# Kernel optimization log

Hardware: AMD Instinct MI355X
Metric: run time of the kernel (lower is better)

Reference implementation:

```python
import jax, jax.numpy as jnp
import numpy as np


def _lstm_cell(x, h, c, Wih, Whh, bih, bhh):
    # PyTorch LSTMCell gate order: i, f, g, o
    g = x @ Wih.T + h @ Whh.T + bih + bhh
    i, f, gg, o = jnp.split(g, 4, axis=-1)
    c = jax.nn.sigmoid(f) * c + jax.nn.sigmoid(i) * jnp.tanh(gg)
    h = jax.nn.sigmoid(o) * jnp.tanh(c)
    return h, c


def setup_inputs() -> dict:
    F, H, B, Te, Td = 64, 128, 1024, 168, 24
    shapes = {
        'input_p_q': (B, Te, F), 'label_p': (B, Td),
        'Wi_w': (H, F), 'Wi_b': (H,), 'We_w': (H, 2 * H),
        'Vd_w': (F, H), 'Vd_b': (F,),
        'enc_Wih': (4 * H, F), 'enc_Whh': (4 * H, H), 'enc_bih': (4 * H,), 'enc_bhh': (4 * H,),
        'mid_Wih': (4 * H, H), 'mid_Whh': (4 * H, H), 'mid_bih': (4 * H,), 'mid_bhh': (4 * H,),
        'Wx_w': (H, H), 'Wx_b': (H,), 'Wh_w': (H, 2 * H),
        'V_w': (1, H), 'V_b': (1,),
        'dec_Wih': (4 * H, H), 'dec_Whh': (4 * H, H), 'dec_bih': (4 * H,), 'dec_bhh': (4 * H,),
        'reg_w': (1, H), 'reg_b': (1,),
    }
    key = jax.random.key(0)
    ks = jax.random.split(key, len(shapes))
    out = {}
    for k, (name, shp) in zip(ks, shapes.items()):
        scale = 1.0 if name in ('input_p_q', 'label_p') else 0.05
        out[name] = jax.random.normal(k, shp, jnp.float32) * scale
    return out


def reference(input_p_q, label_p, Wi_w, Wi_b, We_w, Vd_w, Vd_b,
              enc_Wih, enc_Whh, enc_bih, enc_bhh,
              mid_Wih, mid_Whh, mid_bih, mid_bhh,
              Wx_w, Wx_b, Wh_w, V_w, V_b,
              dec_Wih, dec_Whh, dec_bih, dec_bhh, reg_w, reg_b):
    B, Te, F = input_p_q.shape
    H = Wi_w.shape[0]
    Td = label_p.shape[1]
    h0 = jnp.zeros((B, H), input_p_q.dtype)

    # ---- spatial-attention LSTMCell encoder ----
    xs = jnp.transpose(input_p_q, (1, 0, 2))  # [Te, B, F]

    def enc_step(carry, x_t):
        h, c = carry
        s = jnp.tanh(jnp.concatenate([h, c], axis=1) @ We_w.T
                     + x_t @ Wi_w.T + Wi_b) @ Vd_w.T + Vd_b  # [B, F]
        x_in = x_t * jax.nn.softmax(s, axis=1)
        h, c = _lstm_cell(x_in, h, c, enc_Wih, enc_Whh, enc_bih, enc_bhh)
        return (h, c), h

    _, mid = jax.lax.scan(enc_step, (h0, h0), xs)  # [Te, B, H]

    # ---- single-layer nn.LSTM (LSTM_mid), zero init state ----
    def mid_step(carry, x_t):
        h, c = carry
        h, c = _lstm_cell(x_t, h, c, mid_Wih, mid_Whh, mid_bih, mid_bhh)
        return (h, c), h

    (hi, ci), mid_out = jax.lax.scan(mid_step, (h0, h0), mid)
    mid_out = jnp.transpose(mid_out, (1, 0, 2))  # [B, Te, H]

    # ---- temporal-attention LSTMCell decoder (no softmax on scores, faithful) ----
    wx_mid = mid_out @ Wx_w.T + Wx_b  # [B, Te, H]

    def dec_step(carry, _):
        hi, ci = carry
        q = jnp.concatenate([hi, ci], axis=1) @ Wh_w.T  # [B, H]
        s = jnp.tanh(q[:, None, :] + wx_mid) @ V_w.T + V_b  # [B, Te, 1]
        dec_in = jnp.einsum('bt,bth->bh', s[..., 0], mid_out)
        hi, ci = _lstm_cell(dec_in, hi, ci, dec_Wih, dec_Whh, dec_bih, dec_bhh)
        return (hi, ci), hi

    _, dec = jax.lax.scan(dec_step, (hi, ci), None, length=Td)  # [Td, B, H]
    out = jnp.transpose(dec, (1, 0, 2)) @ reg_w.T + reg_b  # [B, Td, 1]
    return out[..., 0]
```

## Files before the change

kernel.cpp:

```cpp
#include <hip/hip_runtime.h>

#define B_   1024
#define TE   168
#define TD   24
#define F_   64
#define H_   128
#define H2_  256
#define G_   512

#define OFF_WhT    0
#define OFF_dWihT  16384
#define OFF_dWhhT  49152
#define OFF_ENCB   81920
#define OFF_MIDB   82432
#define OFF_DECB   82944
#define OFF_W16    83456
#define W16_We     0
#define W16_Wi     32768
#define W16_Vd     40960
#define W16_eWih   49152
#define W16_eWhh   81920
#define W16_mWih   147456
#define W16_mWhh   212992
#define W16_Wx     278528
#define W16_TOT    294912
#define OFF_MID    230912
#define OFF_WX     (OFF_MID + (B_*TE*H_)/2)
#define OFF_STH    (OFF_WX  + (B_*TE*H_)/2)
#define OFF_STC    (OFF_STH + B_*H_)
#define WS_FLOATS  (OFF_STC + B_*H_)

typedef _Float16 h2 __attribute__((ext_vector_type(2)));
typedef _Float16 h8 __attribute__((ext_vector_type(8)));
typedef _Float16 f16x8 __attribute__((ext_vector_type(8)));
typedef float    f32x4 __attribute__((ext_vector_type(4)));

__device__ __forceinline__ float fexp2(float x) { return __builtin_amdgcn_exp2f(x); }
__device__ __forceinline__ float frcp(float x)  { return __builtin_amdgcn_rcpf(x); }
#define LOG2E 1.4426950408889634f

__device__ __forceinline__ float sigm(float x) {
    return frcp(1.f + fexp2(-LOG2E * x));
}
__device__ __forceinline__ float tanh_fast(float x) {
    float e = fexp2(2.f * LOG2E * x);
    return 1.f - 2.f * frcp(e + 1.f);
}

__device__ __forceinline__ float fdot2(h2 a, h2 b, float c) {
#if __has_builtin(__builtin_amdgcn_fdot2)
    return __builtin_amdgcn_fdot2(a, b, c, false);
#else
    return c + (float)a[0] * (float)b[0] + (float)a[1] * (float)b[1];
#endif
}
__device__ __forceinline__ void fma4(float4& g, const float4 wv, const float s) {
    g.x = __builtin_fmaf(wv.x, s, g.x);
    g.y = __builtin_fmaf(wv.y, s, g.y);
    g.z = __builtin_fmaf(wv.z, s, g.z);
    g.w = __builtin_fmaf(wv.w, s, g.w);
}

#define SH(V,I)  __builtin_shufflevector(V, V, 2*(I), 2*(I)+1)
#define SL(CG)   (4*((CG) + ((CG)>>3)))

#define DPAIR2(LOV, HIV, R0, R1) { \
    h2 c0=SH(LOV,0), c1=SH(LOV,1), c2=SH(LOV,2), c3=SH(LOV,3); \
    h2 c4=SH(HIV,0), c5=SH(HIV,1), c6=SH(HIV,2), c7=SH(HIV,3); \
    a00.x=fdot2(R0,c0,a00.x); a00.y=fdot2(R0,c1,a00.y); a00.z=fdot2(R0,c2,a00.z); a00.w=fdot2(R0,c3,a00.w); \
    a01.x=fdot2(R0,c4,a01.x); a01.y=fdot2(R0,c5,a01.y); a01.z=fdot2(R0,c6,a01.z); a01.w=fdot2(R0,c7,a01.w); \
    a10.x=fdot2(R1,c0,a10.x); a10.y=fdot2(R1,c1,a10.y); a10.z=fdot2(R1,c2,a10.z); a10.w=fdot2(R1,c3,a10.w); \
    a11.x=fdot2(R1,c4,a11.x); a11.y=fdot2(R1,c5,a11.y); a11.z=fdot2(R1,c6,a11.z); a11.w=fdot2(R1,c7,a11.w); \
}

__device__ __forceinline__ f32x4 mfma16(f16x8 a, f16x8 b, f32x4 c) {
    return __builtin_amdgcn_mfma_f32_16x16x32_f16(a, b, c, 0, 0, 0);
}

struct PrepArgs {
    const float *We, *Wi, *Vd, *eWih, *eWhh, *eBih, *eBhh,
                *mWih, *mWhh, *mBih, *mBhh, *Wx, *Wh, *dWih, *dWhh, *dBih, *dBhh;
};

__global__ void prep_kernel(PrepArgs a, float* __restrict__ ws, int* __restrict__ flags) {
    int sec  = blockIdx.x >> 2;
    int base = (blockIdx.x & 3) * blockDim.x + threadIdx.x;
    const int stride = blockDim.x * 4;
    _Float16* w16 = (_Float16*)(ws + OFF_W16);

    if (sec <= 2) {
        const float* src = (sec == 0) ? a.Wh : (sec == 1) ? a.dWih : a.dWhh;
        int R = (sec == 0) ? 128 : 512;
        int C = (sec == 0) ? 256 : 128;
        int off = (sec == 0) ? OFF_WhT : (sec == 1) ? OFF_dWihT : OFF_dWhhT;
        int n = R * C;
        _Float16* hd = (_Float16*)(ws + off);
        for (int o = base; o < n; o += stride) {
            int r = o % R, c = o / R;
            hd[(c >> 1) * 2 * R + 2 * r + (c & 1)] = (_Float16)src[r * C + c];
        }
    } else if (sec == 3) {
        for (int i = base; i < 512; i += stride) ws[OFF_ENCB + i] = a.eBih[i] + a.eBhh[i];
    } else if (sec == 4) {
        for (int i = base; i < 512; i += stride) ws[OFF_MIDB + i] = a.mBih[i] + a.mBhh[i];
    } else if (sec == 5) {
        for (int i = base; i < 512; i += stride) ws[OFF_DECB + i] = a.dBih[i] + a.dBhh[i];
        for (int i = base; i < 64; i += stride) flags[i] = 0;
    } else if (sec <= 13) {
        const int dsto[8] = {W16_We, W16_Wi, W16_Vd, W16_eWih, W16_eWhh, W16_mWih, W16_mWhh, W16_Wx};
        const int cnt[8]  = {32768, 8192, 8192, 32768, 65536, 65536, 65536, 16384};
        const float* srcs[8] = {a.We, a.Wi, a.Vd, a.eWih, a.eWhh, a.mWih, a.mWhh, a.Wx};
        int k = sec - 6;
        const float* s = srcs[k];
        _Float16* d = w16 + dsto[k];
        int n = cnt[k];
        for (int i = base; i < n; i += stride) d[i] = (_Float16)s[i];
    }
}

__global__ __launch_bounds__(512, 1) void enc_mid_kernel(
    const float* __restrict__ x_all,
    const float* __restrict__ Wi_b,
    const float* __restrict__ Vd_b,
    const float* __restrict__ Wx_b,
    float* __restrict__ ws,
    int* __restrict__ flags)
{
    const int tid  = threadIdx.x;
    const int wave = tid >> 6;
    const int lane = tid & 63;
    const int g    = lane >> 4;
    const int cc   = lane & 15;
    const int role = blockIdx.x >> 6;
    const int grp  = blockIdx.x & 63;
    const int b0   = grp * 16;
    const int col  = wave * 16 + cc;
    const _Float16* w16 = (const _Float16*)(ws + OFF_W16);
    _Float16* hencG = (_Float16*)(ws + OFF_MID);

    if (role == 0) {
        __shared__ __align__(16) _Float16 m1In[16][328];
        __shared__ __align__(16) _Float16 encIn[16][200];
        __shared__ __align__(16) _Float16 avT[16][136];
        __shared__ __align__(16) float sS[16][68];
        __shared__ __align__(16) float xf[16][64];
        __shared__ __align__(16) float cE[16][132];
        __shared__ float bWi[H_], bVd[F_], bE[G_];

        for (int i = tid; i < 16 * 328; i += 512) ((_Float16*)m1In)[i]  = (_Float16)0.f;
        for (int i = tid; i < 16 * 200; i += 512) ((_Float16*)encIn)[i] = (_Float16)0.f;
        for (int i = tid; i < 16 * 132; i += 512) ((float*)cE)[i] = 0.f;
        if (tid < H_) bWi[tid] = Wi_b[tid];
        if (tid < F_) bVd[tid] = Vd_b[tid];
        bE[tid] = ws[OFF_ENCB + tid];
        if (tid < 256) {
            int m = tid >> 4, c4 = (tid & 15) * 4;
            float4 v = *(const float4*)&x_all[((size_t)(b0 + m) * TE + 0) * F_ + c4];
            *(float4*)&xf[m][c4] = v;
            m1In[m][256 + c4]     = (_Float16)v.x;
            m1In[m][256 + c4 + 1] = (_Float16)v.y;
            m1In[m][256 + c4 + 2] = (_Float16)v.z;
            m1In[m][256 + c4 + 3] = (_Float16)v.w;
        }

        f16x8 wWe[8], wWi[2], wVd[4], wIh[4][2], wHh[4][4];
        {
            const _Float16* p = w16 + W16_We + (size_t)col * 256 + 8 * g;
            #pragma unroll
            for (int ks = 0; ks < 8; ++ks) wWe[ks] = *(const f16x8*)(p + ks * 32);
            const _Float16* p2 = w16 + W16_Wi + (size_t)col * 64 + 8 * g;
            wWi[0] = *(const f16x8*)(p2);
            wWi[1] = *(const f16x8*)(p2 + 32);
            if (wave < 4) {
                const _Float16* p3 = w16 + W16_Vd + (size_t)col * 128 + 8 * g;
                #pragma unroll
                for (int ks = 0; ks < 4; ++ks) wVd[ks] = *(const f16x8*)(p3 + ks * 32);
            } else {
                #pragma unroll
                for (int ks = 0; ks < 4; ++ks) wVd[ks] = f16x8{};
            }
            #pragma unroll
            for (int q = 0; q < 4; ++q) {
                const _Float16* pi = w16 + W16_eWih + (size_t)(q * 128 + col) * 64 + 8 * g;
                wIh[q][0] = *(const f16x8*)(pi);
                wIh[q][1] = *(const f16x8*)(pi + 32);
                const _Float16* ph = w16 + W16_eWhh + (size_t)(q * 128 + col) * 128 + 8 * g;
                #pragma unroll
                for (int ks = 0; ks < 4; ++ks) wHh[q][ks] = *(const f16x8*)(ph + ks * 32);
            }
        }
        __syncthreads();

        float4 xr = make_float4(0.f, 0.f, 0.f, 0.f);

        for (int t = 0; t < TE; ++t) {
            {
                f16x8 aF[10];
                #pragma unroll
                for (int ks = 0; ks < 10; ++ks)
                    aF[ks] = *(const f16x8*)&m1In[cc][ks * 32 + 8 * g];
                f32x4 acc = {0.f, 0.f, 0.f, 0.f};
                #pragma unroll
                for (int ks = 0; ks < 8; ++ks)
                    acc = mfma16(aF[ks], wWe[ks], acc);
                acc = mfma16(aF[8], wWi[0], acc);
                acc = mfma16(aF[9], wWi[1], acc);
                float bw = bWi[col];
                #pragma unroll
                for (int r = 0; r < 4; ++r)
                    avT[4 * g + r][col] = (_Float16)tanh_fast(acc[r] + bw);
            }
            __syncthreads();

            if (wave < 4) {
                f16x8 aF[4];
                #pragma unroll
                for (int ks = 0; ks < 4; ++ks)
                    aF[ks] = *(const f16x8*)&avT[cc][ks * 32 + 8 * g];
                f32x4 acc = {0.f, 0.f, 0.f, 0.f};
                #pragma unroll
                for (int ks = 0; ks < 4; ++ks)
                    acc = mfma16(aF[ks], wVd[ks], acc);
                float bv = bVd[col];
                #pragma unroll
                for (int r = 0; r < 4; ++r)
                    sS[4 * g + r][col] = acc[r] + bv;
            } else if (t + 1 < TE) {
                int q = tid - 256, m = q >> 4, c4 = (q & 15) * 4;
                xr = *(const float4*)&x_all[((size_t)(b0 + m) * TE + (t + 1)) * F_ + c4];
            }
            __syncthreads();

            {
                int m = tid >> 5, c = tid & 31;
                float v0 = sS[m][c], v1 = sS[m][c + 32];
                float mx = fmaxf(v0, v1);
                #pragma unroll
                for (int off = 16; off > 0; off >>= 1) mx = fmaxf(mx, __shfl_xor(mx, off, 64));
                float e0 = fexp2((v0 - mx) * LOG2E);
                float e1 = fexp2((v1 - mx) * LOG2E);
                float sm = e0 + e1;
                #pragma unroll
                for (int off = 16; off > 0; off >>= 1) sm += __shfl_xor(sm, off, 64);
                float rs = frcp(sm);
                encIn[m][c]      = (_Float16)(xf[m][c]      * e0 * rs);
                encIn[m][c + 32] = (_Float16)(xf[m][c + 32] * e1 * rs);
            }
            __syncthreads();

            f32x4 ge[4];
            {
                f16x8 aF[6];
                #pragma unroll
                for (int ks = 0; ks < 6; ++ks)
                    aF[ks] = *(const f16x8*)&encIn[cc][ks * 32 + 8 * g];
                #pragma unroll
                for (int q = 0; q < 4; ++q) {
                    f32x4 acc = {0.f, 0.f, 0.f, 0.f};
                    acc = mfma16(aF[0], wIh[q][0], acc);
                    acc = mfma16(aF[1], wIh[q][1], acc);
                    #pragma unroll
                    for (int ks = 0; ks < 4; ++ks)
                        acc = mfma16(aF[2 + ks], wHh[q][ks], acc);
                    ge[q] = acc;
                }
            }
            __syncthreads();
            {
                float bi = bE[col], bf = bE[col + 128], bg = bE[col + 256], bo = bE[col + 384];
                #pragma unroll
                for (int r = 0; r < 4; ++r) {
                    int m = 4 * g + r;
                    float gi = ge[0][r] + bi, gf = ge[1][r] + bf,
                          gg = ge[2][r] + bg, go = ge[3][r] + bo;
                    float cn = sigm(gf) * cE[m][col] + sigm(gi) * tanh_fast(gg);
                    float h  = sigm(go) * tanh_fast(cn);
                    cE[m][col] = cn;
                    _Float16 hh = (_Float16)h;
                    encIn[m][64 + col] = hh;
                    m1In[m][col]       = hh;
                    m1In[m][128 + col] = (_Float16)cn;
                    hencG[((size_t)(b0 + m) * TE + t) * H_ + col] = hh;
                }
                if (tid >= 256 && t + 1 < TE) {
                    int q = tid - 256, m = q >> 4, c4 = (q & 15) * 4;
                    *(float4*)&xf[m][c4] = xr;
                    m1In[m][256 + c4]     = (_Float16)xr.x;
                    m1In[m][256 + c4 + 1] = (_Float16)xr.y;
                    m1In[m][256 + c4 + 2] = (_Float16)xr.z;
                    m1In[m][256 + c4 + 3] = (_Float16)xr.w;
                }
            }
            __syncthreads();
            if (((t + 1) & 7) == 0 && tid == 0)
                __hip_atomic_store(flags + grp, t + 1, __ATOMIC_RELEASE, __HIP_MEMORY_SCOPE_AGENT);
        }
    } else {
        __shared__ __align__(16) _Float16 midIn[16][264];
        __shared__ __align__(16) float cM[16][132];
        __shared__ float bM[G_], bWx[H_];

        for (int i = tid; i < 16 * 264; i += 512) ((_Float16*)midIn)[i] = (_Float16)0.f;
        for (int i = tid; i < 16 * 132; i += 512) ((float*)cM)[i] = 0.f;
        if (tid < H_) bWx[tid] = Wx_b[tid];
        bM[tid] = ws[OFF_MIDB + tid];

        f16x8 wIhB[4][4], wHhB[4][4], wWx[4];
        {
            #pragma unroll
            for (int q = 0; q < 4; ++q) {
                const _Float16* pi = w16 + W16_mWih + (size_t)(q * 128 + col) * 128 + 8 * g;
                const _Float16* ph = w16 + W16_mWhh + (size_t)(q * 128 + col) * 128 + 8 * g;
                #pragma unroll
                for (int ks = 0; ks < 4; ++ks) {
                    wIhB[q][ks] = *(const f16x8*)(pi + ks * 32);
                    wHhB[q][ks] = *(const f16x8*)(ph + ks * 32);
                }
            }
            const _Float16* px = w16 + W16_Wx + (size_t)col * 128 + 8 * g;
            #pragma unroll
            for (int ks = 0; ks < 4; ++ks) wWx[ks] = *(const f16x8*)(px + ks * 32);
        }
        _Float16* wxH = (_Float16*)(ws + OFF_WX);
        __syncthreads();

        if (tid == 0) {
            while (__hip_atomic_load(flags + grp, __ATOMIC_ACQUIRE, __HIP_MEMORY_SCOPE_AGENT) < 8)
                __builtin_amdgcn_s_sleep(4);
        }
        __syncthreads();
        if (tid < 256) {
            int m = tid >> 4, s8 = (tid & 15) * 8;
            *(f16x8*)&midIn[m][s8] = *(const f16x8*)&hencG[((size_t)(b0 + m) * TE + 0) * H_ + s8];
        }
        __syncthreads();

        f16x8 hpre = {};
        f32x4 accx = {0.f, 0.f, 0.f, 0.f};

        for (int t = 0; t < TE; ++t) {
            const bool pre_ok = (t + 1 < TE) && (((t + 1) & 7) != 0);
            f32x4 gm[4];
            {
                f16x8 aF[8];
                #pragma unroll
                for (int ks = 0; ks < 8; ++ks)
                    aF[ks] = *(const f16x8*)&midIn[cc][ks * 32 + 8 * g];
                #pragma unroll
                for (int q = 0; q < 4; ++q) {
                    f32x4 acc = {0.f, 0.f, 0.f, 0.f};
                    #pragma unroll
                    for (int ks = 0; ks < 4; ++ks)
                        acc = mfma16(aF[ks], wIhB[q][ks], acc);
                    #pragma unroll
                    for (int ks = 0; ks < 4; ++ks)
                        acc = mfma16(aF[4 + ks], wHhB[q][ks], acc);
                    gm[q] = acc;
                }
                if (t > 0) {
                    f32x4 acc = {0.f, 0.f, 0.f, 0.f};
                    #pragma unroll
                    for (int ks = 0; ks < 4; ++ks)
                        acc = mfma16(aF[4 + ks], wWx[ks], acc);
                    accx = acc;
                }
            }
            if (tid < 256 && pre_ok) {
                int m = tid >> 4, s8 = (tid & 15) * 8;
                hpre = *(const f16x8*)&hencG[((size_t)(b0 + m) * TE + (t + 1)) * H_ + s8];
            }
            __syncthreads();

            {
                float bi = bM[col], bf = bM[col + 128], bg = bM[col + 256], bo = bM[col + 384];
                float bw = bWx[col];
                #pragma unroll
                for (int r = 0; r < 4; ++r) {
                    int m = 4 * g + r;
                    float gi = gm[0][r] + bi, gf = gm[1][r] + bf,
                          gg = gm[2][r] + bg, go = gm[3][r] + bo;
                    float cn = sigm(gf) * cM[m][col] + sigm(gi) * tanh_fast(gg);
                    float h  = sigm(go) * tanh_fast(cn);
                    cM[m][col] = cn;
                    _Float16 hh = (_Float16)h;
                    midIn[m][128 + col] = hh;
                    hencG[((size_t)(b0 + m) * TE + t) * H_ + col] = hh;
                    if (t > 0)
                        wxH[((size_t)(b0 + m) * TE + (t - 1)) * H_ + col] = (_Float16)(accx[r] + bw);
                }
                if (tid < 256 && pre_ok) {
                    int m = tid >> 4, s8 = (tid & 15) * 8;
                    *(f16x8*)&midIn[m][s8] = hpre;
                }
            }
            __syncthreads();

            if (t + 1 < TE && ((t + 1) & 7) == 0) {
                if (tid == 0) {
                    while (__hip_atomic_load(flags + grp, __ATOMIC_ACQUIRE, __HIP_MEMORY_SCOPE_AGENT) < t + 9)
                        __builtin_amdgcn_s_sleep(4);
                }
                __syncthreads();
                if (tid < 256) {
                    int m = tid >> 4, s8 = (tid & 15) * 8;
                    *(f16x8*)&midIn[m][s8] = *(const f16x8*)&hencG[((size_t)(b0 + m) * TE + (t + 1)) * H_ + s8];
                }
                __syncthreads();
            }
        }

        {
            f16x8 ax[4];
            #pragma unroll
            for (int ks = 0; ks < 4; ++ks)
                ax[ks] = *(const f16x8*)&midIn[cc][128 + ks * 32 + 8 * g];
            f32x4 acc = {0.f, 0.f, 0.f, 0.f};
            #pragma unroll
            for (int ks = 0; ks < 4; ++ks)
                acc = mfma16(ax[ks], wWx[ks], acc);
            float bw = bWx[col];
            #pragma unroll
            for (int r = 0; r < 4; ++r) {
                int m = 4 * g + r;
                wxH[((size_t)(b0 + m) * TE + (TE - 1)) * H_ + col] = (_Float16)(acc[r] + bw);
            }
        }
        for (int idx = tid; idx < 2048; idx += 512) {
            int m = idx >> 7, j = idx & 127;
            ws[OFF_STH + (b0 + m) * H_ + j] = (float)midIn[m][128 + j];
            ws[OFF_STC + (b0 + m) * H_ + j] = cM[m][j];
        }
    }
}

#define QP_ 132

__global__ __launch_bounds__(512, 2) void dec_kernel(
    const float* __restrict__ Vw_in,
    const float* __restrict__ Vb_in,
    const float* __restrict__ rw_in,
    const float* __restrict__ rb_in,
    const float* __restrict__ ws,
    float* __restrict__ out)
{
    __shared__ __align__(16) float scr[9216];
    __shared__ __align__(16) float hc2[2][H2_];
    __shared__ __align__(16) float qv[2][QP_];
    __shared__ __align__(16) float sb[2][TE];
    __shared__ __align__(16) float dinp[8][2][H_];
    __shared__ float bD[G_], Vw[H_], rw[H_];

    const int tid = threadIdx.x;
    const int b0  = blockIdx.x * 2;
    const float Vb = Vb_in[0], rb = rb_in[0];

    {
        int r = tid >> 8, c = tid & 255;
        hc2[r][c] = (c < H_) ? ws[OFF_STH + (b0 + r) * H_ + c]
                             : ws[OFF_STC + (b0 + r) * H_ + (c - H_)];
    }
    if (tid < H_) { Vw[tid] = Vw_in[tid]; rw[tid] = rw_in[tid]; }
    bD[tid] = ws[OFF_DECB + tid];
    __syncthreads();

    const h8* WhH2  = (const h8*)(ws + OFF_WhT);
    const h8* dWih2 = (const h8*)(ws + OFF_dWihT);
    const h8* dWhh2 = (const h8*)(ws + OFF_dWhhT);
    const h8* wx8   = (const h8*)(ws + OFF_WX);
    typedef _Float16 h4 __attribute__((ext_vector_type(4)));
    const h4* mid4 = (const h4*)(ws + OFF_MID);

    for (int td = 0; td < TD; ++td) {
        {
            int cg = tid & 15, ks = tid >> 4;
            int p0 = ks * 4;
            float4 a00 = make_float4(0.f,0.f,0.f,0.f), a01 = a00, a10 = a00, a11 = a00;
            #pragma unroll
            for (int i = 0; i < 4; ++i) {
                int p = p0 + i;
                h8 lo = WhH2[p * 32 + cg * 2];
                h8 hi = WhH2[p * 32 + cg * 2 + 1];
                h2 r0; r0[0] = (_Float16)hc2[0][2*p]; r0[1] = (_Float16)hc2[0][2*p+1];
                h2 r1; r1[0] = (_Float16)hc2[1][2*p]; r1[1] = (_Float16)hc2[1][2*p+1];
                DPAIR2(lo, hi, r0, r1);
            }
            int sl = SL(cg);
            float* sp = scr + ks * 288;
            *(float4*)(sp +       sl) = a00; *(float4*)(sp +  72 + sl) = a01;
            *(float4*)(sp + 144 + sl) = a10; *(float4*)(sp + 216 + sl) = a11;
        }
        __syncthreads();
        if (tid < 256) {
            int j = tid & 127, r = tid >> 7;
            int e = j & 7, cgj = j >> 3;
            int idx = r * 144 + ((e < 4) ? SL(cgj) + e : 72 + SL(cgj) + (e - 4));
            float v = 0.f;
            #pragma unroll
            for (int ks = 0; ks < 32; ++ks) v += scr[ks * 288 + idx];
            qv[r][j] = v;
        }
        __syncthreads();

        for (int task = tid; task < 2 * TE; task += 512) {
            int r = (task >= TE) ? 1 : 0;
            int tp = task - r * TE;
            const h8* wxr = wx8 + ((size_t)(b0 + r) * TE + tp) * 16;
            float acc = Vb;
            #pragma unroll 4
            for (int kk = 0; kk < 16; ++kk) {
                h8 hv = wxr[kk];
                int j = kk * 8;
                float4 q0 = *(const float4*)&qv[r][j], q1 = *(const float4*)&qv[r][j + 4];
                float4 v0 = *(const float4*)&Vw[j],    v1 = *(const float4*)&Vw[j + 4];
                acc += tanh_fast(q0.x + (float)hv[0]) * v0.x + tanh_fast(q0.y + (float)hv[1]) * v0.y
                     + tanh_fast(q0.z + (float)hv[2]) * v0.z + tanh_fast(q0.w + (float)hv[3]) * v0.w;
                acc += tanh_fast(q1.x + (float)hv[4]) * v1.x + tanh_fast(q1.y + (float)hv[5]) * v1.y
                     + tanh_fast(q1.z + (float)hv[6]) * v1.z + tanh_fast(q1.w + (float)hv[7]) * v1.w;
            }
            sb[r][tp] = acc;
        }
        __syncthreads();

        {
            int ts = tid >> 6, r = (tid >> 5) & 1, cg = tid & 31;
            int t0 = ts * 21;
            float4 a = make_float4(0.f, 0.f, 0.f, 0.f);
            #pragma unroll 3
            for (int tp = t0; tp < t0 + 21; ++tp) {
                float s = sb[r][tp];
                h4 m = mid4[((size_t)(b0 + r) * TE + tp) * 32 + cg];
                float4 mf;
                mf.x = (float)m[0]; mf.y = (float)m[1]; mf.z = (float)m[2]; mf.w = (float)m[3];
                fma4(a, mf, s);
            }
            *(float4*)&dinp[ts][r][cg * 4] = a;
        }
        __syncthreads();
        if (tid < 256) {
            int j = tid & 127, r = tid >> 7;
            qv[r][j] = ((dinp[0][r][j] + dinp[1][r][j]) + (dinp[2][r][j] + dinp[3][r][j]))
                     + ((dinp[4][r][j] + dinp[5][r][j]) + (dinp[6][r][j] + dinp[7][r][j]));
        }
        __syncthreads();

        {
            int cg = tid & 63, ks = tid >> 6;
            int p0 = ks * 8;
            float4 a00 = make_float4(0.f,0.f,0.f,0.f), a01 = a00, a10 = a00, a11 = a00;
            #pragma unroll 4
            for (int i = 0; i < 8; ++i) {
                int p = p0 + i;
                h8 lo = dWih2[p * 128 + cg * 2];
                h8 hi = dWih2[p * 128 + cg * 2 + 1];
                h2 r0; r0[0] = (_Float16)qv[0][2*p]; r0[1] = (_Float16)qv[0][2*p+1];
                h2 r1; r1[0] = (_Float16)qv[1][2*p]; r1[1] = (_Float16)qv[1][2*p+1];
                DPAIR2(lo, hi, r0, r1);
            }
            #pragma unroll 4
            for (int i = 0; i < 8; ++i) {
                int p = p0 + i;
                h8 lo = dWhh2[p * 128 + cg * 2];
                h8 hi = dWhh2[p * 128 + cg * 2 + 1];
                h2 r0; r0[0] = (_Float16)hc2[0][2*p]; r0[1] = (_Float16)hc2[0][2*p+1];
                h2 r1; r1[0] = (_Float16)hc2[1][2*p]; r1[1] = (_Float16)hc2[1][2*p+1];
                DPAIR2(lo, hi, r0, r1);
            }
            int sl = SL(cg);
            float* sp = scr + ks * 1152;
            *(float4*)(sp +       sl) = a00; *(float4*)(sp + 288 + sl) = a01;
            *(float4*)(sp + 576 + sl) = a10; *(float4*)(sp + 864 + sl) = a11;
        }
        __syncthreads();

        if (tid < 256) {
            int j = tid & 127, r = tid >> 7;
            int e = j & 7, cgj = j >> 3;
            int i0, i1, i2, i3;
            {
                int c0 = cgj, c1 = 16 + cgj, c2 = 32 + cgj, c3 = 48 + cgj;
                i0 = (e < 4) ? SL(c0) + e : 288 + SL(c0) + (e - 4);
                i1 = (e < 4) ? SL(c1) + e : 288 + SL(c1) + (e - 4);
                i2 = (e < 4) ? SL(c2) + e : 288 + SL(c2) + (e - 4);
                i3 = (e < 4) ? SL(c3) + e : 288 + SL(c3) + (e - 4);
            }
            const float* sp = scr + r * 576;
            float gi = bD[j], gf = bD[j + 128], gg = bD[j + 256], go = bD[j + 384];
            #pragma unroll
            for (int ks = 0; ks < 8; ++ks) {
                const float* p = sp + ks * 1152;
                gi += p[i0]; gf += p[i1]; gg += p[i2]; go += p[i3];
            }
            float c = sigm(gf) * hc2[r][H_ + j] + sigm(gi) * tanh_fast(gg);
            float h = sigm(go) * tanh_fast(c);
            hc2[r][H_ + j] = c; hc2[r][j] = h;
        }
        __syncthreads();

        if (tid < 128) {
            int r = tid >> 6, lane = tid & 63;
            float v = hc2[r][lane] * rw[lane] + hc2[r][lane + 64] * rw[lane + 64];
            for (int off = 32; off > 0; off >>= 1) v += __shfl_xor(v, off, 64);
            if (lane == 0) out[(b0 + r) * TD + td] = v + rb;
        }
    }
}

extern "C" void kernel_launch(void* const* d_in, const int* in_sizes, int n_in,
                              void* d_out, int out_size, void* d_ws, size_t ws_size,
                              hipStream_t stream)
{
    (void)in_sizes; (void)n_in; (void)out_size;
    if (ws_size < (size_t)WS_FLOATS * sizeof(float)) return;

    const float* x_all = (const float*)d_in[0];
    const float* Wi_b  = (const float*)d_in[3];
    const float* Vd_b  = (const float*)d_in[6];
    const float* Wx_b  = (const float*)d_in[16];
    const float* V_w   = (const float*)d_in[18];
    const float* V_b   = (const float*)d_in[19];
    const float* reg_w = (const float*)d_in[24];
    const float* reg_b = (const float*)d_in[25];
    float* ws  = (float*)d_ws;
    float* out = (float*)d_out;
    int* flags = (int*)d_out;

    PrepArgs pa{
        (const float*)d_in[4],
        (const float*)d_in[2],
        (const float*)d_in[5],
        (const float*)d_in[7],
        (const float*)d_in[8],
        (const float*)d_in[9],
        (const float*)d_in[10],
        (const float*)d_in[11],
        (const float*)d_in[12],
        (const float*)d_in[13],
        (const float*)d_in[14],
        (const float*)d_in[15],
        (const float*)d_in[17],
        (const float*)d_in[20],
        (const float*)d_in[21],
        (const float*)d_in[22],
        (const float*)d_in[23]
    };

    prep_kernel<<<56, 256, 0, stream>>>(pa, ws, flags);
    enc_mid_kernel<<<128, 512, 0, stream>>>(x_all, Wi_b, Vd_b, Wx_b, ws, flags);
    dec_kernel<<<512, 512, 0, stream>>>(V_w, V_b, reg_w, reg_b, ws, out);
}
```

Baseline: 1.079 ms.

## Fuse attention softmax into Vd MFMA waves and double-buffer encoder input

Result: slower. 1.395 ms (+29.3%).

```diff
diff --git a/kernel.cpp b/kernel.cpp
--- a/kernel.cpp
+++ b/kernel.cpp
@@ -140,15 +140,14 @@
 
     if (role == 0) {
         __shared__ __align__(16) _Float16 m1In[16][328];
-        __shared__ __align__(16) _Float16 encIn[16][200];
+        __shared__ __align__(16) _Float16 encIn[2][16][200];
         __shared__ __align__(16) _Float16 avT[16][136];
-        __shared__ __align__(16) float sS[16][68];
         __shared__ __align__(16) float xf[16][64];
         __shared__ __align__(16) float cE[16][132];
         __shared__ float bWi[H_], bVd[F_], bE[G_];
 
         for (int i = tid; i < 16 * 328; i += 512) ((_Float16*)m1In)[i]  = (_Float16)0.f;
-        for (int i = tid; i < 16 * 200; i += 512) ((_Float16*)encIn)[i] = (_Float16)0.f;
+        for (int i = tid; i < 2 * 16 * 200; i += 512) ((_Float16*)encIn)[i] = (_Float16)0.f;
         for (int i = tid; i < 16 * 132; i += 512) ((float*)cE)[i] = 0.f;
         if (tid < H_) bWi[tid] = Wi_b[tid];
         if (tid < F_) bVd[tid] = Vd_b[tid];
@@ -163,7 +162,7 @@
             m1In[m][256 + c4 + 3] = (_Float16)v.w;
         }
 
-        f16x8 wWe[8], wWi[2], wVd[4], wIh[4][2], wHh[4][4];
+        f16x8 wWe[8], wWi[2], wVd[4][4], wIh[4][2], wHh[4][4];
         {
             const _Float16* p = w16 + W16_We + (size_t)col * 256 + 8 * g;
             #pragma unroll
@@ -172,12 +171,17 @@
             wWi[0] = *(const f16x8*)(p2);
             wWi[1] = *(const f16x8*)(p2 + 32);
             if (wave < 4) {
-                const _Float16* p3 = w16 + W16_Vd + (size_t)col * 128 + 8 * g;
-                #pragma unroll
-                for (int ks = 0; ks < 4; ++ks) wVd[ks] = *(const f16x8*)(p3 + ks * 32);
+                #pragma unroll
+                for (int nt = 0; nt < 4; ++nt) {
+                    const _Float16* p3 = w16 + W16_Vd + (size_t)(nt * 16 + cc) * 128 + 8 * g;
+                    #pragma unroll
+                    for (int ks = 0; ks < 4; ++ks) wVd[nt][ks] = *(const f16x8*)(p3 + ks * 32);
+                }
             } else {
                 #pragma unroll
-                for (int ks = 0; ks < 4; ++ks) wVd[ks] = f16x8{};
+                for (int nt = 0; nt < 4; ++nt)
+                    #pragma unroll
+                    for (int ks = 0; ks < 4; ++ks) wVd[nt][ks] = f16x8{};
             }
             #pragma unroll
             for (int q = 0; q < 4; ++q) {
@@ -194,6 +198,7 @@
         float4 xr = make_float4(0.f, 0.f, 0.f, 0.f);
 
         for (int t = 0; t < TE; ++t) {
+            const int buf = t & 1;
             {
                 f16x8 aF[10];
                 #pragma unroll
@@ -217,43 +222,43 @@
                 #pragma unroll
                 for (int ks = 0; ks < 4; ++ks)
                     aF[ks] = *(const f16x8*)&avT[cc][ks * 32 + 8 * g];
-                f32x4 acc = {0.f, 0.f, 0.f, 0.f};
-                #pragma unroll
-                for (int ks = 0; ks < 4; ++ks)
-                    acc = mfma16(aF[ks], wVd[ks], acc);
-                float bv = bVd[col];
-                #pragma unroll
-                for (int r = 0; r < 4; ++r)
-                    sS[4 * g + r][col] = acc[r] + bv;
+                f32x4 sA0 = {0.f,0.f,0.f,0.f}, sA1 = sA0, sA2 = sA0, sA3 = sA0;
+                #pragma unroll
+                for (int ks = 0; ks < 4; ++ks) {
+                    sA0 = mfma16(aF[ks], wVd[0][ks], sA0);
+                    sA1 = mfma16(aF[ks], wVd[1][ks], sA1);
+                    sA2 = mfma16(aF[ks], wVd[2][ks], sA2);
+                    sA3 = mfma16(aF[ks], wVd[3][ks], sA3);
+                }
+                float bv0 = bVd[cc], bv1 = bVd[16 + cc], bv2 = bVd[32 + cc], bv3 = bVd[48 + cc];
+                #pragma unroll
+                for (int r = 0; r < 4; ++r) {
+                    float s0 = sA0[r] + bv0, s1 = sA1[r] + bv1, s2 = sA2[r] + bv2, s3 = sA3[r] + bv3;
+                    float mx = fmaxf(fmaxf(s0, s1), fmaxf(s2, s3));
+                    #pragma unroll
+                    for (int off = 8; off > 0; off >>= 1) mx = fmaxf(mx, __shfl_xor(mx, off, 16));
+                    float e0 = fexp2((s0 - mx) * LOG2E), e1 = fexp2((s1 - mx) * LOG2E);
+                    float e2 = fexp2((s2 - mx) * LOG2E), e3 = fexp2((s3 - mx) * LOG2E);
+                    float sm = (e0 + e1) + (e2 + e3);
+                    #pragma unroll
+                    for (int off = 8; off > 0; off >>= 1) sm += __shfl_xor(sm, off, 16);
+                    float rs = frcp(sm);
+                    float ew = (wave == 0) ? e0 : (wave == 1) ? e1 : (wave == 2) ? e2 : e3;
+                    int m = 4 * g + r;
+                    encIn[buf][m][col] = (_Float16)(xf[m][col] * ew * rs);
+                }
             } else if (t + 1 < TE) {
                 int q = tid - 256, m = q >> 4, c4 = (q & 15) * 4;
                 xr = *(const float4*)&x_all[((size_t)(b0 + m) * TE + (t + 1)) * F_ + c4];
             }
             __syncthreads();
 
-            {
-                int m = tid >> 5, c = tid & 31;
-                float v0 = sS[m][c], v1 = sS[m][c + 32];
-                float mx = fmaxf(v0, v1);
-                #pragma unroll
-                for (int off = 16; off > 0; off >>= 1) mx = fmaxf(mx, __shfl_xor(mx, off, 64));
-                float e0 = fexp2((v0 - mx) * LOG2E);
-                float e1 = fexp2((v1 - mx) * LOG2E);
-                float sm = e0 + e1;
-                #pragma unroll
-                for (int off = 16; off > 0; off >>= 1) sm += __shfl_xor(sm, off, 64);
-                float rs = frcp(sm);
-                encIn[m][c]      = (_Float16)(xf[m][c]      * e0 * rs);
-                encIn[m][c + 32] = (_Float16)(xf[m][c + 32] * e1 * rs);
-            }
-            __syncthreads();
-
             f32x4 ge[4];
             {
                 f16x8 aF[6];
                 #pragma unroll
                 for (int ks = 0; ks < 6; ++ks)
-                    aF[ks] = *(const f16x8*)&encIn[cc][ks * 32 + 8 * g];
+                    aF[ks] = *(const f16x8*)&encIn[buf][cc][ks * 32 + 8 * g];
                 #pragma unroll
                 for (int q = 0; q < 4; ++q) {
                     f32x4 acc = {0.f, 0.f, 0.f, 0.f};
@@ -265,7 +270,6 @@
                     ge[q] = acc;
                 }
             }
-            __syncthreads();
             {
                 float bi = bE[col], bf = bE[col + 128], bg = bE[col + 256], bo = bE[col + 384];
                 #pragma unroll
@@ -277,7 +281,7 @@
                     float h  = sigm(go) * tanh_fast(cn);
                     cE[m][col] = cn;
                     _Float16 hh = (_Float16)h;
-                    encIn[m][64 + col] = hh;
+                    encIn[buf ^ 1][m][64 + col] = hh;
                     m1In[m][col]       = hh;
                     m1In[m][128 + col] = (_Float16)cn;
                     hencG[((size_t)(b0 + m) * TE + t) * H_ + col] = hh;
```
